# Performance work log

Measured on AMD Instinct MI355X. Metric: run time of the kernel, lower is better.

The kernel has to match this reference:

```python
import jax, jax.numpy as jnp
import numpy as np

N_HEAD = 16

def setup_inputs() -> dict:
    key = jax.random.key(0)
    k0, k1, k2, k3 = jax.random.split(key, 4)
    S, E, H, T = 2048, 1024, N_HEAD, 4096
    d = E // H
    return {
        "x": jax.random.normal(k0, (S, E), jnp.float32),
        "past": jax.random.normal(k1, (2, H, T, d), jnp.float32),  # stacked [pk, pv]
        "W1": jax.random.normal(k2, (E, 3 * E), jnp.float32) * 0.02,  # c_attn (Conv1D k=1 == linear)
        "b1": jnp.zeros((3 * E,), jnp.float32),
        "W2": jax.random.normal(k3, (E, E), jnp.float32) * 0.02,  # c_proj
        "b2": jnp.zeros((E,), jnp.float32),
        "past_length": 2048,
    }


def reference(x, past, W1, b1, W2, b2, past_length):
    H = N_HEAD
    S, E = x.shape
    d = E // H

    c = x @ W1 + b1  # [S, 3E]
    q, k, v = jnp.split(c, 3, axis=1)

    def split_heads(t):  # [S, E] -> [H, S, d]
        return jnp.transpose(t.reshape(S, H, d), (1, 0, 2))

    q, k, v = split_heads(q), split_heads(k), split_heads(v)

    pk, pv = past[0], past[1]  # [H, T, d]
    k = jax.lax.dynamic_update_slice_in_dim(pk, k, past_length, axis=1)
    v = jax.lax.dynamic_update_slice_in_dim(pv, v, past_length, axis=1)

    # attention scores [H, S, T]
    w = jnp.einsum('hid,hjd->hij', q, k) / np.sqrt(d)
    ns = k.shape[1]
    i = jnp.arange(S)[:, None]
    j = jnp.arange(ns)[None, :]
    b = (i >= j - past_length).astype(w.dtype)
    w = w * b - jnp.float32(1e10) * (1 - b)
    w = jax.nn.softmax(w, axis=-1)

    a = jnp.einsum('hij,hjd->hid', w, v)  # [H, S, d]
    # faithful to original: start index clamps to 0 since axis len == S
    a = jax.lax.dynamic_slice_in_dim(a, past_length, S, axis=1)
    a = jnp.transpose(a, (1, 0, 2)).reshape(S, E)  # merge heads

    out = a @ W2 + b2
    new_cache = jnp.stack([k, v], axis=0)
    return out, new_cache
```

## Files before the change

### kernel.cpp

```cpp
#include <hip/hip_runtime.h>
#include <hip/hip_bf16.h>
#include <stdint.h>


#define S_LEN 2048
#define E_DIM 1024
#define NHEAD 16
#define HDIM  64
#define T_LEN 4096
#define PASTL 2048

typedef __bf16 bf16x8 __attribute__((ext_vector_type(8)));
typedef __bf16 bf16x4 __attribute__((ext_vector_type(4)));
typedef float  f32x4  __attribute__((ext_vector_type(4)));

static __device__ __forceinline__ f32x4 mfma_bf16(bf16x8 a, bf16x8 b, f32x4 c) {
  return __builtin_amdgcn_mfma_f32_16x16x32_bf16(a, b, c, 0, 0, 0);
}

static __device__ __forceinline__ unsigned int f2bf(float f) {
  union { float f; unsigned int u; } v; v.f = f;
  unsigned int u = v.u;
  return (u + 0x7fffu + ((u >> 16) & 1u)) >> 16;
}

static __device__ __forceinline__ float bf2f(unsigned short u) {
  union { unsigned int u; float f; } v; v.u = (unsigned int)u << 16;
  return v.f;
}

#define GLOBAL_LOAD_LDS16(gptr, lptr)                                              \
  __builtin_amdgcn_global_load_lds(                                                \
      (const __attribute__((address_space(1))) unsigned int*)(gptr),               \
      (__attribute__((address_space(3))) unsigned int*)(lptr), 16, 0, 0)


__global__ void prep_kernel(const float* __restrict__ past,
                            const float* __restrict__ x,
                            float* __restrict__ cache,
                            unsigned short* __restrict__ kb,
                            unsigned short* __restrict__ xb) {
  const int n4p = (2 * NHEAD * PASTL * HDIM) / 4;
  const int n4x = (S_LEN * E_DIM) / 4;
  for (int i = blockIdx.x * blockDim.x + threadIdx.x; i < n4p + n4x;
       i += gridDim.x * blockDim.x) {
    if (i < n4p) {
      int e = i * 4;
      int d = e & 63;
      int t = (e >> 6) & (PASTL - 1);
      int hh = (e >> 17) & (NHEAD - 1);
      int kv = e >> 21;
      size_t full = (((size_t)kv * NHEAD + hh) * T_LEN + t) * HDIM + d;
      float4 v = *(const float4*)(past + full);
      *(float4*)(cache + full) = v;
      if (kv == 0) {
        ushort4 u;
        u.x = f2bf(v.x); u.y = f2bf(v.y); u.z = f2bf(v.z); u.w = f2bf(v.w);
        *(ushort4*)(kb + full) = u;
      }
    } else {
      int j = i - n4p;
      float4 v = ((const float4*)x)[j];
      ushort4 u;
      u.x = f2bf(v.x); u.y = f2bf(v.y); u.z = f2bf(v.z); u.w = f2bf(v.w);
      ((ushort4*)xb)[j] = u;
    }
  }
}

__global__ void transpose_convert_kernel(const float* __restrict__ in,
                                         unsigned short* __restrict__ out,
                                         int rows, int cols) {
  __shared__ float tile[64][65];
  const int c0 = blockIdx.x * 64, r0 = blockIdx.y * 64;
  const int tx = threadIdx.x & 63, ty = threadIdx.x >> 6;
#pragma unroll
  for (int r = 0; r < 64; r += 4)
    tile[r + ty][tx] = in[(size_t)(r0 + r + ty) * cols + c0 + tx];
  __syncthreads();
#pragma unroll
  for (int r = 0; r < 64; r += 4)
    out[(size_t)(c0 + r + ty) * rows + r0 + tx] = f2bf(tile[tx][r + ty]);
}

__global__ void vtrans_kernel(const float* __restrict__ vin,
                              unsigned short* __restrict__ vt) {
  __shared__ float tile[64][65];
  const int h = blockIdx.y;
  const int t0 = blockIdx.x * 64;
  const float* in = vin + (size_t)h * T_LEN * HDIM;
  unsigned short* out = vt + (size_t)h * HDIM * T_LEN;
  const int tx = threadIdx.x & 63, ty = threadIdx.x >> 6;
#pragma unroll
  for (int r = 0; r < 64; r += 4)
    tile[r + ty][tx] = in[(size_t)(t0 + r + ty) * HDIM + tx];
  __syncthreads();
#pragma unroll
  for (int r = 0; r < 64; r += 4)
    out[(size_t)(r + ty) * T_LEN + t0 + tx] = f2bf(tile[tx][r + ty]);
}

template <int MODE>
__global__ __launch_bounds__(256) void gemm_bt_kernel(
    const unsigned short* __restrict__ A, const unsigned short* __restrict__ Bt,
    const float* __restrict__ bias, int K,
    float* __restrict__ out_f32, unsigned short* __restrict__ qb,
    float* __restrict__ cache_k, float* __restrict__ cache_v,
    unsigned short* __restrict__ kb) {
  __shared__ alignas(16) unsigned short As[128 * 64];
  __shared__ alignas(16) unsigned short Bs[128 * 64];
  const int tid = threadIdx.x;
  const int lane = tid & 63;
  const int w = tid >> 6;
  const int wm = w >> 1, wn = w & 1;
  const int m0 = blockIdx.y * 128, n0 = blockIdx.x * 128;

  f32x4 acc[4][4];
#pragma unroll
  for (int i = 0; i < 4; ++i)
#pragma unroll
    for (int j = 0; j < 4; ++j) acc[i][j] = f32x4{0.f, 0.f, 0.f, 0.f};

  const int rbase = w * 8 + (lane >> 3);
  const int sbase = lane & 7;

  for (int k0 = 0; k0 < K; k0 += 64) {
#pragma unroll
    for (int q = 0; q < 4; ++q) {
      int row_l = q * 32 + rbase;
      int slot = sbase ^ (row_l & 7);
      const unsigned short* ga = A + (size_t)(m0 + row_l) * K + k0 + slot * 8;
      const unsigned short* gb = Bt + (size_t)(n0 + row_l) * K + k0 + slot * 8;
      unsigned int ldsOff = (unsigned int)(q * 4096 + w * 1024);
      GLOBAL_LOAD_LDS16(ga, (char*)As + ldsOff);
      GLOBAL_LOAD_LDS16(gb, (char*)Bs + ldsOff);
    }
    __syncthreads();
#pragma unroll
    for (int kk = 0; kk < 2; ++kk) {
      bf16x8 af[4], bfr[4];
#pragma unroll
      for (int mi = 0; mi < 4; ++mi) {
        int row = wm * 64 + mi * 16 + (lane & 15);
        int slot = (kk * 4 + (lane >> 4)) ^ (row & 7);
        af[mi] = *reinterpret_cast<const bf16x8*>((const char*)As + row * 128 + slot * 16);
      }
#pragma unroll
      for (int ni = 0; ni < 4; ++ni) {
        int row = wn * 64 + ni * 16 + (lane & 15);
        int slot = (kk * 4 + (lane >> 4)) ^ (row & 7);
        bfr[ni] = *reinterpret_cast<const bf16x8*>((const char*)Bs + row * 128 + slot * 16);
      }
#pragma unroll
      for (int mi = 0; mi < 4; ++mi)
#pragma unroll
        for (int ni = 0; ni < 4; ++ni)
          acc[mi][ni] = mfma_bf16(af[mi], bfr[ni], acc[mi][ni]);
    }
    __syncthreads();
  }

#pragma unroll
  for (int ni = 0; ni < 4; ++ni) {
    int n = n0 + wn * 64 + ni * 16 + (lane & 15);
    float bv = bias[n];
#pragma unroll
    for (int mi = 0; mi < 4; ++mi) {
#pragma unroll
      for (int r = 0; r < 4; ++r) {
        int m = m0 + wm * 64 + mi * 16 + (lane >> 4) * 4 + r;
        float val = acc[mi][ni][r] + bv;
        if (MODE == 0) {
          if (n < E_DIM) {
            qb[(size_t)m * E_DIM + n] = f2bf(val * 0.18033688f);
          } else if (n < 2 * E_DIM) {
            int e = n - E_DIM;
            size_t idx = ((size_t)(e >> 6) * T_LEN + (PASTL + m)) * HDIM + (e & 63);
            cache_k[idx] = val;
            kb[idx] = f2bf(val);
          } else {
            int e = n - 2 * E_DIM;
            size_t idx = ((size_t)(e >> 6) * T_LEN + (PASTL + m)) * HDIM + (e & 63);
            cache_v[idx] = val;
          }
        } else {
          out_f32[(size_t)m * E_DIM + n] = val;
        }
      }
    }
  }
}

__global__ __launch_bounds__(256) void attn_kernel(
    const unsigned short* __restrict__ qb, const unsigned short* __restrict__ kb,
    const unsigned short* __restrict__ vt,
    unsigned short* __restrict__ o_part, float* __restrict__ l_part) {
  __shared__ alignas(16) unsigned short Ks[2][64 * 64];
  __shared__ alignas(16) unsigned short Vs[2][64 * 64];
  __shared__ alignas(16) __bf16 p_lds[4][32][72];
  const int fid = blockIdx.x;
  const int h = (fid & 7) + ((fid >= 448) ? 8 : 0);
  const int g = (fid >> 3) - ((fid >= 448) ? 56 : 0);
  int x, c;
  if (g < 24) { x = g / 3; c = g - 3 * x; }
  else { int g2 = g - 24; x = 8 + (g2 >> 2); c = g2 & 3; }

  const int tid = threadIdx.x;
  const int w = tid >> 6;
  const int lane = tid & 63;
  const int lr = lane & 15;
  const int lg = lane >> 4;
  const int qb0 = x * 128;
  const int q0 = qb0 + w * 32;

  const unsigned short* qr0 = qb + (size_t)(q0 + lr) * E_DIM + h * HDIM + lg * 8;
  const unsigned short* qr1 = qb + (size_t)(q0 + 16 + lr) * E_DIM + h * HDIM + lg * 8;
  const bf16x8 qf00 = *reinterpret_cast<const bf16x8*>(qr0);
  const bf16x8 qf01 = *reinterpret_cast<const bf16x8*>(qr0 + 32);
  const bf16x8 qf10 = *reinterpret_cast<const bf16x8*>(qr1);
  const bf16x8 qf11 = *reinterpret_cast<const bf16x8*>(qr1 + 32);

  const unsigned short* kh = kb + (size_t)h * T_LEN * HDIM;
  const unsigned short* vh = vt + (size_t)h * HDIM * T_LEN;

  const int srow = tid >> 3;
  const int sseg = (tid & 7) ^ (srow & 7);
  const unsigned short* ksrc = kh + (size_t)srow * HDIM + sseg * 8;
  const unsigned short* vsrc = vh + (size_t)srow * T_LEN + sseg * 8;

  f32x4 o[2][4];
  float lsum[2][2];
#pragma unroll
  for (int sb = 0; sb < 2; ++sb) {
    lsum[sb][0] = lsum[sb][1] = 0.f;
#pragma unroll
    for (int jd = 0; jd < 4; ++jd) o[sb][jd] = f32x4{0.f, 0.f, 0.f, 0.f};
  }

  const int jmaxq = q0 + PASTL;
  const int NTfull = 34 + 2 * x;
  const int tb = c * 16;
  const int te = (tb + 16 < NTfull) ? tb + 16 : NTfull;
  const int NT = te - tb;
  const int tbeg = tb * 64;

  auto stageK = [&](int b, int t0) {
    GLOBAL_LOAD_LDS16(ksrc + (size_t)t0 * HDIM, (char*)Ks[b] + tid * 16);
    GLOBAL_LOAD_LDS16(ksrc + (size_t)(t0 + 32) * HDIM, (char*)Ks[b] + 4096 + tid * 16);
  };
  auto stageV = [&](int b, int t0) {
    GLOBAL_LOAD_LDS16(vsrc + t0, (char*)Vs[b] + tid * 16);
    GLOBAL_LOAD_LDS16(vsrc + t0 + (size_t)32 * T_LEN, (char*)Vs[b] + 4096 + tid * 16);
  };

  stageK(0, tbeg);
  stageV(0, tbeg);
  int cur = 0;
  int t0 = tbeg;
  for (int i = 0; i < NT; ++i, t0 += 64) {
    const bool more = (i + 1 < NT);
    asm volatile("s_waitcnt vmcnt(2)" ::: "memory");
    __builtin_amdgcn_s_barrier();
    __builtin_amdgcn_sched_barrier(0);
    if (more) stageK(cur ^ 1, t0 + 64);

    bf16x8 kf[4][2];
#pragma unroll
    for (int j = 0; j < 4; ++j) {
      int row = j * 16 + lr;
      int s0 = lg ^ (row & 7), s1 = (4 + lg) ^ (row & 7);
      kf[j][0] = *reinterpret_cast<const bf16x8*>((const char*)Ks[cur] + row * 128 + s0 * 16);
      kf[j][1] = *reinterpret_cast<const bf16x8*>((const char*)Ks[cur] + row * 128 + s1 * 16);
    }

    f32x4 sc[2][4];
#pragma unroll
    for (int sb = 0; sb < 2; ++sb)
#pragma unroll
      for (int j = 0; j < 4; ++j) sc[sb][j] = f32x4{0.f, 0.f, 0.f, 0.f};
    __builtin_amdgcn_s_setprio(1);
#pragma unroll
    for (int j = 0; j < 4; ++j) {
      sc[0][j] = mfma_bf16(kf[j][0], qf00, sc[0][j]);
      sc[0][j] = mfma_bf16(kf[j][1], qf01, sc[0][j]);
      sc[1][j] = mfma_bf16(kf[j][0], qf10, sc[1][j]);
      sc[1][j] = mfma_bf16(kf[j][1], qf11, sc[1][j]);
    }
    __builtin_amdgcn_s_setprio(0);

    const bool partial = (t0 + 63 > jmaxq);
    const int thr = q0 + PASTL - t0 + lr;
    const int lg4 = lg * 4;
#pragma unroll
    for (int sb = 0; sb < 2; ++sb) {
#pragma unroll
      for (int j = 0; j < 4; ++j) {
        bf16x4 pk;
#pragma unroll
        for (int r = 0; r < 4; ++r) {
          float p = __builtin_amdgcn_exp2f(sc[sb][j][r]);
          if (partial && (j * 16 + lg4 + r > thr + sb * 16)) p = 0.f;
          lsum[sb][r >> 1] += p;
          pk[r] = (__bf16)p;
        }
        *reinterpret_cast<bf16x4*>(&p_lds[w][sb * 16 + lr][j * 16 + lg4]) = pk;
      }
    }
    bf16x8 pa[2][2];
#pragma unroll
    for (int sb = 0; sb < 2; ++sb) {
      pa[sb][0] = *reinterpret_cast<const bf16x8*>(&p_lds[w][sb * 16 + lr][lg * 8]);
      pa[sb][1] = *reinterpret_cast<const bf16x8*>(&p_lds[w][sb * 16 + lr][32 + lg * 8]);
    }

    if (more) {
      asm volatile("s_waitcnt vmcnt(2)" ::: "memory");
    } else {
      asm volatile("s_waitcnt vmcnt(0)" ::: "memory");
    }
    __builtin_amdgcn_s_barrier();
    __builtin_amdgcn_sched_barrier(0);
    if (more) stageV(cur ^ 1, t0 + 64);

    __builtin_amdgcn_s_setprio(1);
#pragma unroll
    for (int jd = 0; jd < 4; ++jd) {
      int row = jd * 16 + lr;
      int s0 = lg ^ (row & 7), s1 = (4 + lg) ^ (row & 7);
      bf16x8 vf0 = *reinterpret_cast<const bf16x8*>((const char*)Vs[cur] + row * 128 + s0 * 16);
      bf16x8 vf1 = *reinterpret_cast<const bf16x8*>((const char*)Vs[cur] + row * 128 + s1 * 16);
      o[0][jd] = mfma_bf16(pa[0][0], vf0, o[0][jd]);
      o[0][jd] = mfma_bf16(pa[0][1], vf1, o[0][jd]);
      o[1][jd] = mfma_bf16(pa[1][0], vf0, o[1][jd]);
      o[1][jd] = mfma_bf16(pa[1][1], vf1, o[1][jd]);
    }
    __builtin_amdgcn_s_setprio(0);
    cur ^= 1;
  }

  unsigned short* op = o_part + ((size_t)(c * NHEAD + h) * S_LEN) * HDIM;
  float* lp = l_part + (size_t)(c * NHEAD + h) * S_LEN;
#pragma unroll
  for (int sb = 0; sb < 2; ++sb) {
    float ls = lsum[sb][0] + lsum[sb][1];
    ls += __shfl_xor(ls, 16);
    ls += __shfl_xor(ls, 32);
    if (lg == 0) lp[q0 + sb * 16 + lr] = ls;
#pragma unroll
    for (int jd = 0; jd < 4; ++jd) {
#pragma unroll
      for (int r = 0; r < 4; ++r) {
        int row = q0 + sb * 16 + lg * 4 + r;
        op[(size_t)row * HDIM + jd * 16 + lr] = f2bf(o[sb][jd][r]);
      }
    }
  }
}

__global__ __launch_bounds__(256) void attn_merge_kernel(
    const unsigned short* __restrict__ o_part, const float* __restrict__ l_part,
    unsigned short* __restrict__ ab) {
  const int flat = blockIdx.x * 256 + threadIdx.x;
  const int d4 = flat & 15;
  const int row = (flat >> 4) & (S_LEN - 1);
  const int h = flat >> 15;
  const int nc = (row < 1024) ? 3 : 4;
  const size_t cstride_o = (size_t)NHEAD * S_LEN * HDIM;
  const size_t base_o = (((size_t)h * S_LEN) + row) * HDIM + d4 * 4;
  float acc[4] = {0.f, 0.f, 0.f, 0.f};
  float l = 0.f;
  for (int cc = 0; cc < nc; ++cc) {
    ushort4 u = *(const ushort4*)(o_part + cc * cstride_o + base_o);
    acc[0] += bf2f(u.x); acc[1] += bf2f(u.y);
    acc[2] += bf2f(u.z); acc[3] += bf2f(u.w);
    l += l_part[(size_t)cc * NHEAD * S_LEN + (size_t)h * S_LEN + row];
  }
  float inv = 1.f / l;
  ushort4 u;
  u.x = f2bf(acc[0] * inv);
  u.y = f2bf(acc[1] * inv);
  u.z = f2bf(acc[2] * inv);
  u.w = f2bf(acc[3] * inv);
  *(ushort4*)(ab + (size_t)row * E_DIM + h * HDIM + d4 * 4) = u;
}


extern "C" void kernel_launch(void* const* d_in, const int* in_sizes, int n_in,
                              void* d_out, int out_size, void* d_ws, size_t ws_size,
                              hipStream_t stream) {
  (void)in_sizes; (void)n_in; (void)out_size; (void)ws_size;
  const float* x    = (const float*)d_in[0];
  const float* past = (const float*)d_in[1];
  const float* W1   = (const float*)d_in[2];
  const float* b1   = (const float*)d_in[3];
  const float* W2   = (const float*)d_in[4];
  const float* b2   = (const float*)d_in[5];

  float* out = (float*)d_out;
  float* cache_k = out + (size_t)S_LEN * E_DIM;
  float* cache_v = cache_k + (size_t)NHEAD * T_LEN * HDIM;

  char* ws = (char*)d_ws;
  unsigned short* xb  = (unsigned short*)(ws);
  unsigned short* ab  = (unsigned short*)(ws);
  unsigned short* w1t = (unsigned short*)(ws + (size_t)(4u  << 20));
  unsigned short* vt  = (unsigned short*)(ws + (size_t)(4u  << 20));
  unsigned short* w2t = (unsigned short*)(ws + (size_t)(12u << 20));
  unsigned short* qb  = (unsigned short*)(ws + (size_t)(14u << 20));
  unsigned short* kb  = (unsigned short*)(ws + (size_t)(18u << 20));
  unsigned short* o_part = (unsigned short*)(ws + (size_t)(26u << 20));
  float* l_part = (float*)(ws + (size_t)(42u << 20));

  prep_kernel<<<2048, 256, 0, stream>>>(past, x, cache_k, kb, xb);
  transpose_convert_kernel<<<dim3(3072 / 64, 1024 / 64), 256, 0, stream>>>(W1, w1t, 1024, 3072);
  transpose_convert_kernel<<<dim3(1024 / 64, 1024 / 64), 256, 0, stream>>>(W2, w2t, 1024, 1024);
  gemm_bt_kernel<0><<<dim3(3072 / 128, 2048 / 128), 256, 0, stream>>>(
      xb, w1t, b1, 1024, nullptr, qb, cache_k, cache_v, kb);
  vtrans_kernel<<<dim3(T_LEN / 64, NHEAD), 256, 0, stream>>>(cache_v, vt);
  attn_kernel<<<dim3(896), 256, 0, stream>>>(qb, kb, vt, o_part, l_part);
  attn_merge_kernel<<<(NHEAD * S_LEN * 16) / 256, 256, 0, stream>>>(o_part, l_part, ab);
  gemm_bt_kernel<1><<<dim3(1024 / 128, 2048 / 128), 256, 0, stream>>>(
      ab, w2t, b2, 1024, out, nullptr, nullptr, nullptr, nullptr);
}
```

Before: 136.2 us.

## Fuse prep, weight transposes and V transpose; write transposed V from QKV GEMM epilogue

Merges the past copy, x conversion, W1/W2 transpose-convert and the past-V transpose into a single prep kernel that dispatches work by block index. The QKV GEMM epilogue now writes the new V rows directly into the transposed bf16 V buffer, so the separate vtrans kernel, which re-read the whole fp32 V cache, is removed. This cuts three kernel launches and one full pass over the V cache. The workspace layout is reshuffled so buffers that are now live at the same time do not overlap, and the epilogue's transposed ushort4 writes are strided across rows, which may coalesce poorly.

```diff
diff --git a/kernel.cpp b/kernel.cpp
--- a/kernel.cpp
+++ b/kernel.cpp
@@ -34,70 +34,76 @@
       (const __attribute__((address_space(1))) unsigned int*)(gptr),               \
       (__attribute__((address_space(3))) unsigned int*)(lptr), 16, 0, 0)
 
-
-__global__ void prep_kernel(const float* __restrict__ past,
-                            const float* __restrict__ x,
-                            float* __restrict__ cache,
-                            unsigned short* __restrict__ kb,
-                            unsigned short* __restrict__ xb) {
-  const int n4p = (2 * NHEAD * PASTL * HDIM) / 4;
-  const int n4x = (S_LEN * E_DIM) / 4;
-  for (int i = blockIdx.x * blockDim.x + threadIdx.x; i < n4p + n4x;
-       i += gridDim.x * blockDim.x) {
-    if (i < n4p) {
-      int e = i * 4;
-      int d = e & 63;
-      int t = (e >> 6) & (PASTL - 1);
-      int hh = (e >> 17) & (NHEAD - 1);
-      int kv = e >> 21;
-      size_t full = (((size_t)kv * NHEAD + hh) * T_LEN + t) * HDIM + d;
-      float4 v = *(const float4*)(past + full);
-      *(float4*)(cache + full) = v;
-      if (kv == 0) {
+__global__ __launch_bounds__(256) void prep_kernel(
+    const float* __restrict__ past, const float* __restrict__ x,
+    const float* __restrict__ W1, const float* __restrict__ W2,
+    float* __restrict__ cache, unsigned short* __restrict__ kb,
+    unsigned short* __restrict__ xb, unsigned short* __restrict__ w1t,
+    unsigned short* __restrict__ w2t, unsigned short* __restrict__ vtb) {
+  __shared__ float tile[64][65];
+  const int bid = blockIdx.x;
+  const int tid = threadIdx.x;
+  const int tx = tid & 63, ty = tid >> 6;
+
+  if (bid < 512) {
+    const int h = bid >> 5;
+    const int t0 = (bid & 31) * 64;
+    const float* in = past + (size_t)(NHEAD + h) * T_LEN * HDIM;
+    unsigned short* outp = vtb + (size_t)h * HDIM * T_LEN;
+#pragma unroll
+    for (int r = 0; r < 64; r += 4)
+      tile[r + ty][tx] = in[(size_t)(t0 + r + ty) * HDIM + tx];
+    __syncthreads();
+#pragma unroll
+    for (int r = 0; r < 64; r += 4)
+      outp[(size_t)(r + ty) * T_LEN + t0 + tx] = f2bf(tile[tx][r + ty]);
+  } else if (bid < 1536) {
+    const float* in;
+    unsigned short* outp;
+    int rows, cols, c0, r0;
+    if (bid < 1280) {
+      int u = bid - 512;
+      in = W1; outp = w1t; rows = 1024; cols = 3072;
+      c0 = (u % 48) * 64; r0 = (u / 48) * 64;
+    } else {
+      int u = bid - 1280;
+      in = W2; outp = w2t; rows = 1024; cols = 1024;
+      c0 = (u & 15) * 64; r0 = (u >> 4) * 64;
+    }
+#pragma unroll
+    for (int r = 0; r < 64; r += 4)
+      tile[r + ty][tx] = in[(size_t)(r0 + r + ty) * cols + c0 + tx];
+    __syncthreads();
+#pragma unroll
+    for (int r = 0; r < 64; r += 4)
+      outp[(size_t)(c0 + r + ty) * rows + r0 + tx] = f2bf(tile[tx][r + ty]);
+  } else {
+    const int n4p = (2 * NHEAD * PASTL * HDIM) / 4;
+    const int n4x = (S_LEN * E_DIM) / 4;
+    for (int i = (bid - 1536) * 256 + tid; i < n4p + n4x; i += 2048 * 256) {
+      if (i < n4p) {
+        int e = i * 4;
+        int d = e & 63;
+        int t = (e >> 6) & (PASTL - 1);
+        int hh = (e >> 17) & (NHEAD - 1);
+        int kv = e >> 21;
+        size_t full = (((size_t)kv * NHEAD + hh) * T_LEN + t) * HDIM + d;
+        float4 v = *(const float4*)(past + full);
+        *(float4*)(cache + full) = v;
+        if (kv == 0) {
+          ushort4 u;
+          u.x = f2bf(v.x); u.y = f2bf(v.y); u.z = f2bf(v.z); u.w = f2bf(v.w);
+          *(ushort4*)(kb + full) = u;
+        }
+      } else {
+        int j = i - n4p;
+        float4 v = ((const float4*)x)[j];
         ushort4 u;
         u.x = f2bf(v.x); u.y = f2bf(v.y); u.z = f2bf(v.z); u.w = f2bf(v.w);
-        *(ushort4*)(kb + full) = u;
-      }
-    } else {
-      int j = i - n4p;
-      float4 v = ((const float4*)x)[j];
-      ushort4 u;
-      u.x = f2bf(v.x); u.y = f2bf(v.y); u.z = f2bf(v.z); u.w = f2bf(v.w);
-      ((ushort4*)xb)[j] = u;
-    }
-  }
-}
-
-__global__ void transpose_convert_kernel(const float* __restrict__ in,
-                                         unsigned short* __restrict__ out,
-                                         int rows, int cols) {
-  __shared__ float tile[64][65];
-  const int c0 = blockIdx.x * 64, r0 = blockIdx.y * 64;
-  const int tx = threadIdx.x & 63, ty = threadIdx.x >> 6;
-#pragma unroll
-  for (int r = 0; r < 64; r += 4)
-    tile[r + ty][tx] = in[(size_t)(r0 + r + ty) * cols + c0 + tx];
-  __syncthreads();
-#pragma unroll
-  for (int r = 0; r < 64; r += 4)
-    out[(size_t)(c0 + r + ty) * rows + r0 + tx] = f2bf(tile[tx][r + ty]);
-}
-
-__global__ void vtrans_kernel(const float* __restrict__ vin,
-                              unsigned short* __restrict__ vt) {
-  __shared__ float tile[64][65];
-  const int h = blockIdx.y;
-  const int t0 = blockIdx.x * 64;
-  const float* in = vin + (size_t)h * T_LEN * HDIM;
-  unsigned short* out = vt + (size_t)h * HDIM * T_LEN;
-  const int tx = threadIdx.x & 63, ty = threadIdx.x >> 6;
-#pragma unroll
-  for (int r = 0; r < 64; r += 4)
-    tile[r + ty][tx] = in[(size_t)(t0 + r + ty) * HDIM + tx];
-  __syncthreads();
-#pragma unroll
-  for (int r = 0; r < 64; r += 4)
-    out[(size_t)(r + ty) * T_LEN + t0 + tx] = f2bf(tile[tx][r + ty]);
+        ((ushort4*)xb)[j] = u;
+      }
+    }
+  }
 }
 
 template <int MODE>
@@ -106,7 +112,7 @@
     const float* __restrict__ bias, int K,
     float* __restrict__ out_f32, unsigned short* __restrict__ qb,
     float* __restrict__ cache_k, float* __restrict__ cache_v,
-    unsigned short* __restrict__ kb) {
+    unsigned short* __restrict__ kb, unsigned short* __restrict__ vtb) {
   __shared__ alignas(16) unsigned short As[128 * 64];
   __shared__ alignas(16) unsigned short Bs[128 * 64];
   const int tid = threadIdx.x;
@@ -166,26 +172,38 @@
     float bv = bias[n];
 #pragma unroll
     for (int mi = 0; mi < 4; ++mi) {
-#pragma unroll
-      for (int r = 0; r < 4; ++r) {
-        int m = m0 + wm * 64 + mi * 16 + (lane >> 4) * 4 + r;
-        float val = acc[mi][ni][r] + bv;
-        if (MODE == 0) {
-          if (n < E_DIM) {
-            qb[(size_t)m * E_DIM + n] = f2bf(val * 0.18033688f);
-          } else if (n < 2 * E_DIM) {
-            int e = n - E_DIM;
-            size_t idx = ((size_t)(e >> 6) * T_LEN + (PASTL + m)) * HDIM + (e & 63);
-            cache_k[idx] = val;
-            kb[idx] = f2bf(val);
-          } else {
-            int e = n - 2 * E_DIM;
-            size_t idx = ((size_t)(e >> 6) * T_LEN + (PASTL + m)) * HDIM + (e & 63);
-            cache_v[idx] = val;
+      int mbase = m0 + wm * 64 + mi * 16 + (lane >> 4) * 4;
+      float v4[4];
+#pragma unroll
+      for (int r = 0; r < 4; ++r) v4[r] = acc[mi][ni][r] + bv;
+      if (MODE == 0) {
+        if (n < E_DIM) {
+#pragma unroll
+          for (int r = 0; r < 4; ++r)
+            qb[(size_t)(mbase + r) * E_DIM + n] = f2bf(v4[r] * 0.18033688f);
+        } else if (n < 2 * E_DIM) {
+          int e = n - E_DIM;
+          size_t base = ((size_t)(e >> 6) * T_LEN + (PASTL + mbase)) * HDIM + (e & 63);
+#pragma unroll
+          for (int r = 0; r < 4; ++r) {
+            cache_k[base + (size_t)r * HDIM] = v4[r];
+            kb[base + (size_t)r * HDIM] = f2bf(v4[r]);
           }
         } else {
-          out_f32[(size_t)m * E_DIM + n] = val;
+          int e = n - 2 * E_DIM;
+          int hh = e >> 6, d = e & 63;
+          size_t base = ((size_t)hh * T_LEN + (PASTL + mbase)) * HDIM + d;
+#pragma unroll
+          for (int r = 0; r < 4; ++r) cache_v[base + (size_t)r * HDIM] = v4[r];
+          ushort4 u;
+          u.x = f2bf(v4[0]); u.y = f2bf(v4[1]);
+          u.z = f2bf(v4[2]); u.w = f2bf(v4[3]);
+          *(ushort4*)(vtb + ((size_t)hh * HDIM + d) * T_LEN + PASTL + mbase) = u;
         }
+      } else {
+#pragma unroll
+        for (int r = 0; r < 4; ++r)
+          out_f32[(size_t)(mbase + r) * E_DIM + n] = v4[r];
       }
     }
   }
@@ -401,24 +419,22 @@
   float* cache_v = cache_k + (size_t)NHEAD * T_LEN * HDIM;
 
   char* ws = (char*)d_ws;
-  unsigned short* xb  = (unsigned short*)(ws);
-  unsigned short* ab  = (unsigned short*)(ws);
-  unsigned short* w1t = (unsigned short*)(ws + (size_t)(4u  << 20));
-  unsigned short* vt  = (unsigned short*)(ws + (size_t)(4u  << 20));
-  unsigned short* w2t = (unsigned short*)(ws + (size_t)(12u << 20));
-  unsigned short* qb  = (unsigned short*)(ws + (size_t)(14u << 20));
-  unsigned short* kb  = (unsigned short*)(ws + (size_t)(18u << 20));
+  unsigned short* w2t = (unsigned short*)(ws);
+  unsigned short* qb  = (unsigned short*)(ws + (size_t)(2u  << 20));
+  unsigned short* kb  = (unsigned short*)(ws + (size_t)(6u  << 20));
+  unsigned short* vtb = (unsigned short*)(ws + (size_t)(14u << 20));
+  unsigned short* xb  = (unsigned short*)(ws + (size_t)(22u << 20));
+  unsigned short* ab  = (unsigned short*)(ws + (size_t)(22u << 20));
+  unsigned short* w1t = (unsigned short*)(ws + (size_t)(26u << 20));
   unsigned short* o_part = (unsigned short*)(ws + (size_t)(26u << 20));
   float* l_part = (float*)(ws + (size_t)(42u << 20));
 
-  prep_kernel<<<2048, 256, 0, stream>>>(past, x, cache_k, kb, xb);
-  transpose_convert_kernel<<<dim3(3072 / 64, 1024 / 64), 256, 0, stream>>>(W1, w1t, 1024, 3072);
-  transpose_convert_kernel<<<dim3(1024 / 64, 1024 / 64), 256, 0, stream>>>(W2, w2t, 1024, 1024);
+  prep_kernel<<<3584, 256, 0, stream>>>(past, x, W1, W2, cache_k, kb, xb, w1t,
+                                        w2t, vtb);
   gemm_bt_kernel<0><<<dim3(3072 / 128, 2048 / 128), 256, 0, stream>>>(
-      xb, w1t, b1, 1024, nullptr, qb, cache_k, cache_v, kb);
-  vtrans_kernel<<<dim3(T_LEN / 64, NHEAD), 256, 0, stream>>>(cache_v, vt);
-  attn_kernel<<<dim3(896), 256, 0, stream>>>(qb, kb, vt, o_part, l_part);
+      xb, w1t, b1, 1024, nullptr, qb, cache_k, cache_v, kb, vtb);
+  attn_kernel<<<dim3(896), 256, 0, stream>>>(qb, kb, vtb, o_part, l_part);
   attn_merge_kernel<<<(NHEAD * S_LEN * 16) / 256, 256, 0, stream>>>(o_part, l_part, ab);
   gemm_bt_kernel<1><<<dim3(1024 / 128, 2048 / 128), 256, 0, stream>>>(
-      ab, w2t, b2, 1024, out, nullptr, nullptr, nullptr, nullptr);
-}
+      ab, w2t, b2, 1024, out, nullptr, nullptr, nullptr, nullptr, nullptr);
+}
```

Result: faster. 125.5 us (-7.9%).
